# Performance work log

Measured on AMD Instinct MI355X. Metric: run time of the kernel, lower is better.

## Reference

```python
import jax, jax.numpy as jnp
import numpy as np

D_MODEL = 1024
N_HEADS = 16
HEAD_DIM = D_MODEL // N_HEADS
WINDOW = 256
NEG_INF = -1e30  # finite stand-in for -inf; identical softmax result, NaN-safe


def setup_inputs() -> dict:
    key = jax.random.key(0)
    ks = jax.random.split(key, 5)
    B, L = 1, 4096
    s = 1.0 / np.sqrt(D_MODEL)
    return {
        "x": jax.random.normal(ks[0], (B, L, D_MODEL), dtype=jnp.float32),
        "Wq": jax.random.normal(ks[1], (D_MODEL, D_MODEL), dtype=jnp.float32) * s,
        "Wk": jax.random.normal(ks[2], (D_MODEL, D_MODEL), dtype=jnp.float32) * s,
        "Wv": jax.random.normal(ks[3], (D_MODEL, D_MODEL), dtype=jnp.float32) * s,
        "Wo": jax.random.normal(ks[4], (D_MODEL, D_MODEL), dtype=jnp.float32) * s,
    }


def reference(x, Wq, Wk, Wv, Wo):
    B, L, _ = x.shape
    # projections (nn.Linear applies x @ W.T; weights here are stored as [out,in])
    q = (x @ Wq.T).reshape(B, L, N_HEADS, HEAD_DIM).transpose(0, 2, 1, 3)  # [B,H,L,Dh]
    k = (x @ Wk.T).reshape(B, L, N_HEADS, HEAD_DIM).transpose(0, 2, 1, 3)
    v = (x @ Wv.T).reshape(B, L, N_HEADS, HEAD_DIM).transpose(0, 2, 1, 3)

    # sliding-window causal mask: position i attends to j in [i-WINDOW+1, i]
    i = jnp.arange(L)[:, None]
    j = jnp.arange(L)[None, :]
    allowed = (j <= i) & (j >= i - WINDOW + 1)  # [L,L] bool

    scale = 1.0 / jnp.sqrt(jnp.asarray(HEAD_DIM, dtype=q.dtype))
    scores = jnp.einsum("bhqd,bhkd->bhqk", q, k) * scale  # [B,H,L,L]
    scores = jnp.where(allowed, scores, NEG_INF)
    attn = jax.nn.softmax(scores, axis=-1)
    out = jnp.einsum("bhqk,bhkd->bhqd", attn, v)  # [B,H,L,Dh]
    out = out.transpose(0, 2, 1, 3).reshape(B, L, D_MODEL)
    return out @ Wo.T
```

## Files before the change

kernel.cpp:

```cpp
#include <hip/hip_runtime.h>

using bf16x8 = __attribute__((ext_vector_type(8))) short;
using u16x8  = __attribute__((ext_vector_type(8))) unsigned short;
using f32x4  = __attribute__((ext_vector_type(4))) float;

#define LSEQ   4096
#define NH     16
#define DH     64
#define WIN    256
#define DM     1024

__device__ __forceinline__ void gl2lds16(const void* g, void* l) {
  __builtin_amdgcn_global_load_lds(
      (const __attribute__((address_space(1))) unsigned int*)g,
      (__attribute__((address_space(3))) unsigned int*)l,
      16, 0, 0);
}

__device__ __forceinline__ unsigned short f2bf(float f) {
  unsigned int u = __float_as_uint(f);
  u += 0x7fffu + ((u >> 16) & 1u);
  return (unsigned short)(u >> 16);
}

__global__ __launch_bounds__(256) void cvt_all(
    const float* __restrict__ x,  const float* __restrict__ wq,
    const float* __restrict__ wk, const float* __restrict__ wv,
    const float* __restrict__ wo, unsigned short* __restrict__ dst)
{
  const size_t i = ((size_t)blockIdx.x * 256 + threadIdx.x) * 8;
  const size_t XN = (size_t)LSEQ * DM;
  const float* src;
  size_t off;
  if (i < XN) { src = x; off = i; }
  else {
    const size_t j = i - XN;
    const int s = (int)(j >> 20);
    off = j & ((1u << 20) - 1);
    src = (s == 0) ? wq : (s == 1) ? wk : (s == 2) ? wv : wo;
  }
  const f32x4 f0 = *(const f32x4*)(src + off);
  const f32x4 f1 = *(const f32x4*)(src + off + 4);
  u16x8 o;
  o[0] = f2bf(f0[0]); o[1] = f2bf(f0[1]); o[2] = f2bf(f0[2]); o[3] = f2bf(f0[3]);
  o[4] = f2bf(f1[0]); o[5] = f2bf(f1[1]); o[6] = f2bf(f1[2]); o[7] = f2bf(f1[3]);
  *(u16x8*)(dst + i) = o;
}

__device__ __forceinline__ void gemm_tile(
    const unsigned short* __restrict__ X,
    const unsigned short* __restrict__ W,
    int m0, int n0,
    unsigned short* As, unsigned short* Bs,
    f32x4 (&acc)[4][4])
{
  const int tid  = threadIdx.x;
  const int lane = tid & 63;
  const int wave = tid >> 6;
  const int wm = wave >> 1, wn = wave & 1;
  const int fr = lane & 15, quad = lane >> 4;

  const f32x4 zero = {0.f, 0.f, 0.f, 0.f};
  #pragma unroll
  for (int i = 0; i < 4; ++i)
    #pragma unroll
    for (int j = 0; j < 4; ++j)
      acc[i][j] = zero;

  const unsigned short* ga[4];
  const unsigned short* gb[4];
  char* la[4];
  char* lb[4];
  #pragma unroll
  for (int cc = 0; cc < 4; ++cc) {
    const int c = tid + cc * 256;
    const int row = c >> 3;
    const int gp  = (c & 7) ^ (row & 7);
    ga[cc] = X + (size_t)(m0 + row) * DM + gp * 8;
    gb[cc] = W + (size_t)(n0 + row) * DM + gp * 8;
    la[cc] = (char*)As + c * 16;
    lb[cc] = (char*)Bs + c * 16;
  }

  const int sw = fr & 7;
  for (int kt = 0; kt < DM; kt += 64) {
    #pragma unroll
    for (int cc = 0; cc < 4; ++cc) {
      gl2lds16(ga[cc] + kt, la[cc]);
      gl2lds16(gb[cc] + kt, lb[cc]);
    }
    __syncthreads();

    #pragma unroll
    for (int s = 0; s < 2; ++s) {
      bf16x8 a[4], b[4];
      #pragma unroll
      for (int t = 0; t < 4; ++t)
        a[t] = *(const bf16x8*)(As + (wm * 64 + t * 16 + fr) * 64
                                   + (((s * 4 + quad) ^ sw) * 8));
      #pragma unroll
      for (int t = 0; t < 4; ++t)
        b[t] = *(const bf16x8*)(Bs + (wn * 64 + t * 16 + fr) * 64
                                   + (((s * 4 + quad) ^ sw) * 8));
      #pragma unroll
      for (int i = 0; i < 4; ++i)
        #pragma unroll
        for (int j = 0; j < 4; ++j)
          acc[i][j] = __builtin_amdgcn_mfma_f32_16x16x32_bf16(a[i], b[j], acc[i][j], 0, 0, 0);
    }
    __syncthreads();
  }
}

__global__ __launch_bounds__(256) void proj_gemm(
    const unsigned short* __restrict__ X,
    const unsigned short* __restrict__ Wq,
    const unsigned short* __restrict__ Wk,
    const unsigned short* __restrict__ Wv,
    unsigned short* __restrict__ Qo,
    unsigned short* __restrict__ Ko,
    unsigned short* __restrict__ Vt)
{
  __shared__ unsigned short As[128 * 64];
  __shared__ unsigned short Bs[128 * 64];
  const int id = blockIdx.x;
  const int lane = threadIdx.x & 63;
  const int wave = threadIdx.x >> 6;
  const int wm = wave >> 1, wn = wave & 1;
  const int cn = lane & 15, quad = lane >> 4;
  f32x4 acc[4][4];

  if (id < 512) {
    const int m0   = (id & 31) * 128;
    const int by   = id >> 5;
    const int wsel = by >> 3;
    const int n0   = (by & 7) * 128;
    gemm_tile(X, wsel ? Wk : Wq, m0, n0, As, Bs, acc);

    const float qscl = wsel ? 1.0f : 0.180336881f;
    unsigned short* O = wsel ? Ko : Qo;
    #pragma unroll
    for (int i = 0; i < 4; ++i)
      #pragma unroll
      for (int j = 0; j < 4; ++j)
        #pragma unroll
        for (int r = 0; r < 4; ++r) {
          const int row = m0 + wm * 64 + i * 16 + quad * 4 + r;
          const int col = n0 + wn * 64 + j * 16 + cn;
          const int h = col >> 6, d = col & 63;
          O[(size_t)(h * LSEQ + row) * DH + d] = f2bf(acc[i][j][r] * qscl);
        }
  } else {
    const int vid = id - 512;
    const int m0 = (vid & 7) * 128;
    const int n0 = (vid >> 3) * 128;
    gemm_tile(Wv, X, m0, n0, As, Bs, acc);

    #pragma unroll
    for (int i = 0; i < 4; ++i)
      #pragma unroll
      for (int j = 0; j < 4; ++j)
        #pragma unroll
        for (int r = 0; r < 4; ++r) {
          const int row = m0 + wm * 64 + i * 16 + quad * 4 + r;
          const int col = n0 + wn * 64 + j * 16 + cn;
          Vt[(size_t)row * LSEQ + col] = f2bf(acc[i][j][r]);
        }
  }
}

__global__ __launch_bounds__(256) void out_gemm(
    const unsigned short* __restrict__ X,
    const unsigned short* __restrict__ W,
    float* __restrict__ O)
{
  __shared__ unsigned short As2[64 * 64];
  __shared__ unsigned short Bs[128 * 64];
  const int m0 = blockIdx.x * 64;
  const int n0 = blockIdx.y * 128;
  const int tid  = threadIdx.x;
  const int lane = tid & 63;
  const int wave = tid >> 6;
  const int wm = wave >> 1, wn = wave & 1;
  const int fr = lane & 15, quad = lane >> 4;

  const f32x4 zero = {0.f, 0.f, 0.f, 0.f};
  f32x4 acc[2][4];
  #pragma unroll
  for (int i = 0; i < 2; ++i)
    #pragma unroll
    for (int j = 0; j < 4; ++j)
      acc[i][j] = zero;

  const unsigned short* ga[2];
  char* la[2];
  #pragma unroll
  for (int cc = 0; cc < 2; ++cc) {
    const int c = tid + cc * 256;
    const int row = c >> 3;
    const int gp  = (c & 7) ^ (row & 7);
    ga[cc] = X + (size_t)(m0 + row) * DM + gp * 8;
    la[cc] = (char*)As2 + c * 16;
  }
  const unsigned short* gb[4];
  char* lb[4];
  #pragma unroll
  for (int cc = 0; cc < 4; ++cc) {
    const int c = tid + cc * 256;
    const int row = c >> 3;
    const int gp  = (c & 7) ^ (row & 7);
    gb[cc] = W + (size_t)(n0 + row) * DM + gp * 8;
    lb[cc] = (char*)Bs + c * 16;
  }

  const int sw = fr & 7;
  for (int kt = 0; kt < DM; kt += 64) {
    #pragma unroll
    for (int cc = 0; cc < 2; ++cc)
      gl2lds16(ga[cc] + kt, la[cc]);
    #pragma unroll
    for (int cc = 0; cc < 4; ++cc)
      gl2lds16(gb[cc] + kt, lb[cc]);
    __syncthreads();

    #pragma unroll
    for (int s = 0; s < 2; ++s) {
      bf16x8 a[2], b[4];
      #pragma unroll
      for (int t = 0; t < 2; ++t)
        a[t] = *(const bf16x8*)(As2 + (wm * 32 + t * 16 + fr) * 64
                                    + (((s * 4 + quad) ^ sw) * 8));
      #pragma unroll
      for (int t = 0; t < 4; ++t)
        b[t] = *(const bf16x8*)(Bs + (wn * 64 + t * 16 + fr) * 64
                                   + (((s * 4 + quad) ^ sw) * 8));
      #pragma unroll
      for (int i = 0; i < 2; ++i)
        #pragma unroll
        for (int j = 0; j < 4; ++j)
          acc[i][j] = __builtin_amdgcn_mfma_f32_16x16x32_bf16(a[i], b[j], acc[i][j], 0, 0, 0);
    }
    __syncthreads();
  }

  const int cn = lane & 15;
  #pragma unroll
  for (int i = 0; i < 2; ++i)
    #pragma unroll
    for (int j = 0; j < 4; ++j)
      #pragma unroll
      for (int r = 0; r < 4; ++r) {
        const int row = m0 + wm * 32 + i * 16 + quad * 4 + r;
        const int col = n0 + wn * 64 + j * 16 + cn;
        O[(size_t)row * DM + col] = acc[i][j][r];
      }
}

#define PSTR 72
__global__ __launch_bounds__(512) void attn_fwd(
    const unsigned short* __restrict__ Q,
    const unsigned short* __restrict__ K,
    const unsigned short* __restrict__ Vt,
    unsigned short* __restrict__ Oa)
{
  __shared__ unsigned short Ks[2][64 * PSTR];
  __shared__ unsigned short Vs[2][64 * PSTR];
  __shared__ unsigned short Pl[8][16 * PSTR];
  const int id   = blockIdx.x;
  const int h    = (id & 7) | ((id >> 8) << 3);
  const int bq0  = ((id >> 3) & 31) * 128;
  const int tid  = threadIdx.x;
  const int wave = tid >> 6;
  const int lane = tid & 63;
  const int n = lane & 15, quad = lane >> 4;
  const int q0 = bq0 + wave * 16;
  unsigned short* pl = Pl[wave];

  const size_t qbase = ((size_t)(h * LSEQ + q0 + n)) * DH + quad * 8;
  const bf16x8 aq0 = *(const bf16x8*)(Q + qbase);
  const bf16x8 aq1 = *(const bf16x8*)(Q + qbase + 32);

  const int lo = (bq0 >= WIN) ? (bq0 - WIN) : 0;
  const int hi = bq0 + 128;

  const int krow = tid >> 3, part = tid & 7;
  const size_t kg = ((size_t)(h * LSEQ + krow)) * DH + part * 8;
  const size_t vg = ((size_t)(h * DH + krow)) * LSEQ + part * 8;
  const int ld = krow * PSTR + part * 8;

  {
    *(bf16x8*)(Ks[0] + ld) = *(const bf16x8*)(K  + kg + (size_t)lo * DH);
    *(bf16x8*)(Vs[0] + ld) = *(const bf16x8*)(Vt + vg + lo);
  }
  __syncthreads();

  const f32x4 zero = {0.f, 0.f, 0.f, 0.f};
  f32x4 acc[4] = {zero, zero, zero, zero};
  float li[4] = {0.f, 0.f, 0.f, 0.f};

  int t = 0;
  for (int jb = lo; jb < hi; jb += 64, ++t) {
    const int buf = t & 1;
    const bool more = (jb + 64 < hi);
    bf16x8 nk, nv;
    if (more) {
      nk = *(const bf16x8*)(K  + kg + (size_t)(jb + 64) * DH);
      nv = *(const bf16x8*)(Vt + vg + (jb + 64));
    }
    const bool active = (jb <= q0 + 15) && (jb + 63 >= q0 - (WIN - 1));
    if (active) {
      const unsigned short* ks = Ks[buf];
      const unsigned short* vs = Vs[buf];
      f32x4 s[4];
      __builtin_amdgcn_s_setprio(1);
      #pragma unroll
      for (int u = 0; u < 4; ++u) {
        const bf16x8 kb0 = *(const bf16x8*)(ks + (u * 16 + n) * PSTR + quad * 8);
        const bf16x8 kb1 = *(const bf16x8*)(ks + (u * 16 + n) * PSTR + 32 + quad * 8);
        f32x4 c = zero;
        c = __builtin_amdgcn_mfma_f32_16x16x32_bf16(aq0, kb0, c, 0, 0, 0);
        c = __builtin_amdgcn_mfma_f32_16x16x32_bf16(aq1, kb1, c, 0, 0, 0);
        s[u] = c;
      }
      __builtin_amdgcn_s_setprio(0);
      const bool nomask = (jb + 63 <= q0) && (jb >= q0 + 15 - (WIN - 1));
      if (nomask) {
        #pragma unroll
        for (int u = 0; u < 4; ++u)
          #pragma unroll
          for (int r = 0; r < 4; ++r) {
            const float e = __builtin_exp2f(s[u][r] - 32.0f);
            s[u][r] = e;
            li[r] += e;
          }
      } else {
        #pragma unroll
        for (int u = 0; u < 4; ++u)
          #pragma unroll
          for (int r = 0; r < 4; ++r) {
            const int qi = q0 + quad * 4 + r;
            const int kj = jb + u * 16 + n;
            const bool ok = (kj <= qi) && (kj + WIN > qi);
            const float e = __builtin_exp2f(ok ? s[u][r] - 32.0f : -1e30f);
            s[u][r] = e;
            li[r] += e;
          }
      }
      #pragma unroll
      for (int u = 0; u < 4; ++u)
        #pragma unroll
        for (int r = 0; r < 4; ++r)
          pl[(quad * 4 + r) * PSTR + u * 16 + n] = f2bf(s[u][r]);
      asm volatile("s_waitcnt lgkmcnt(0)" ::: "memory");
      const bf16x8 pa0 = *(const bf16x8*)(pl + n * PSTR + quad * 8);
      const bf16x8 pa1 = *(const bf16x8*)(pl + n * PSTR + 32 + quad * 8);
      __builtin_amdgcn_s_setprio(1);
      #pragma unroll
      for (int ct = 0; ct < 4; ++ct) {
        const bf16x8 vb0 = *(const bf16x8*)(vs + (ct * 16 + n) * PSTR + quad * 8);
        const bf16x8 vb1 = *(const bf16x8*)(vs + (ct * 16 + n) * PSTR + 32 + quad * 8);
        acc[ct] = __builtin_amdgcn_mfma_f32_16x16x32_bf16(pa0, vb0, acc[ct], 0, 0, 0);
        acc[ct] = __builtin_amdgcn_mfma_f32_16x16x32_bf16(pa1, vb1, acc[ct], 0, 0, 0);
      }
      __builtin_amdgcn_s_setprio(0);
    }
    if (more) {
      *(bf16x8*)(Ks[buf ^ 1] + ld) = nk;
      *(bf16x8*)(Vs[buf ^ 1] + ld) = nv;
    }
    __syncthreads();
  }

  float rd[4];
  #pragma unroll
  for (int r = 0; r < 4; ++r) {
    float v = li[r];
    v += __shfl_xor(v, 1);
    v += __shfl_xor(v, 2);
    v += __shfl_xor(v, 4);
    v += __shfl_xor(v, 8);
    rd[r] = 1.0f / v;
  }
  #pragma unroll
  for (int ct = 0; ct < 4; ++ct)
    #pragma unroll
    for (int r = 0; r < 4; ++r) {
      const int row = q0 + quad * 4 + r;
      const int col = h * DH + ct * 16 + n;
      Oa[(size_t)row * DM + col] = f2bf(acc[ct][r] * rd[r]);
    }
}

extern "C" void kernel_launch(void* const* d_in, const int* in_sizes, int n_in,
                              void* d_out, int out_size, void* d_ws, size_t ws_size,
                              hipStream_t stream) {
  const float* x  = (const float*)d_in[0];
  const float* Wq = (const float*)d_in[1];
  const float* Wk = (const float*)d_in[2];
  const float* Wv = (const float*)d_in[3];
  const float* Wo = (const float*)d_in[4];
  float* out = (float*)d_out;

  unsigned short* xb  = (unsigned short*)d_ws;
  unsigned short* Wqb = xb  + (size_t)LSEQ * DM;
  unsigned short* Wkb = Wqb + (size_t)DM * DM;
  unsigned short* Wvb = Wkb + (size_t)DM * DM;
  unsigned short* Wob = Wvb + (size_t)DM * DM;
  unsigned short* Q    = Wob + (size_t)DM * DM;
  unsigned short* K    = Q   + (size_t)LSEQ * DM;
  unsigned short* Vt   = K   + (size_t)LSEQ * DM;
  unsigned short* Attn = Vt  + (size_t)LSEQ * DM;

  cvt_all<<<dim3(4096), 256, 0, stream>>>(x, Wq, Wk, Wv, Wo, xb);
  proj_gemm<<<dim3(768), 256, 0, stream>>>(xb, Wqb, Wkb, Wvb, Q, K, Vt);
  attn_fwd<<<dim3(512), 512, 0, stream>>>(Q, K, Vt, Attn);
  out_gemm<<<dim3(64, 8), 256, 0, stream>>>(Attn, Wob, out);
}
```

Baseline: 154.4 us.

## Rewrite projection GEMM as 8-wave 256x256 tiles with double-buffered LDS pipeline

After: 155.3 us. About the same (+0.5%).

```diff
diff --git a/kernel.cpp b/kernel.cpp
--- a/kernel.cpp
+++ b/kernel.cpp
@@ -47,124 +47,189 @@
   *(u16x8*)(dst + i) = o;
 }
 
-__device__ __forceinline__ void gemm_tile(
+#define TS 16384
+
+#define RD_A(f, s, P) (*(const bf16x8*)(Ab + (P) + (wm*128 + (f)*16 + fr)*64 + ((((s)*4+quad) ^ swz)*8)))
+#define RD_B(g, s, P) (*(const bf16x8*)(Bb + (P) + (wn*64  + (g)*16 + fr)*64 + ((((s)*4+quad) ^ swz)*8)))
+
+#define QUAD16(fs, gs)                                                         \
+  do {                                                                         \
+    __builtin_amdgcn_s_setprio(1);                                             \
+    _Pragma("unroll")                                                          \
+    for (int f_ = 0; f_ < 4; ++f_)                                             \
+      _Pragma("unroll")                                                        \
+      for (int g_ = 0; g_ < 2; ++g_)                                           \
+        _Pragma("unroll")                                                      \
+        for (int s_ = 0; s_ < 2; ++s_)                                         \
+          acc[(fs)+f_][(gs)+g_] = __builtin_amdgcn_mfma_f32_16x16x32_bf16(     \
+              a[(fs)+f_][s_], b[(gs)+g_][s_], acc[(fs)+f_][(gs)+g_], 0, 0, 0); \
+    __builtin_amdgcn_s_setprio(0);                                             \
+  } while (0)
+
+__global__ __launch_bounds__(512, 2) void proj8(
     const unsigned short* __restrict__ X,
-    const unsigned short* __restrict__ W,
-    int m0, int n0,
-    unsigned short* As, unsigned short* Bs,
-    f32x4 (&acc)[4][4])
-{
-  const int tid  = threadIdx.x;
-  const int lane = tid & 63;
-  const int wave = tid >> 6;
-  const int wm = wave >> 1, wn = wave & 1;
-  const int fr = lane & 15, quad = lane >> 4;
-
-  const f32x4 zero = {0.f, 0.f, 0.f, 0.f};
-  #pragma unroll
-  for (int i = 0; i < 4; ++i)
-    #pragma unroll
-    for (int j = 0; j < 4; ++j)
-      acc[i][j] = zero;
-
-  const unsigned short* ga[4];
-  const unsigned short* gb[4];
-  char* la[4];
-  char* lb[4];
-  #pragma unroll
-  for (int cc = 0; cc < 4; ++cc) {
-    const int c = tid + cc * 256;
-    const int row = c >> 3;
-    const int gp  = (c & 7) ^ (row & 7);
-    ga[cc] = X + (size_t)(m0 + row) * DM + gp * 8;
-    gb[cc] = W + (size_t)(n0 + row) * DM + gp * 8;
-    la[cc] = (char*)As + c * 16;
-    lb[cc] = (char*)Bs + c * 16;
-  }
-
-  const int sw = fr & 7;
-  for (int kt = 0; kt < DM; kt += 64) {
-    #pragma unroll
-    for (int cc = 0; cc < 4; ++cc) {
-      gl2lds16(ga[cc] + kt, la[cc]);
-      gl2lds16(gb[cc] + kt, lb[cc]);
-    }
-    __syncthreads();
-
-    #pragma unroll
-    for (int s = 0; s < 2; ++s) {
-      bf16x8 a[4], b[4];
-      #pragma unroll
-      for (int t = 0; t < 4; ++t)
-        a[t] = *(const bf16x8*)(As + (wm * 64 + t * 16 + fr) * 64
-                                   + (((s * 4 + quad) ^ sw) * 8));
-      #pragma unroll
-      for (int t = 0; t < 4; ++t)
-        b[t] = *(const bf16x8*)(Bs + (wn * 64 + t * 16 + fr) * 64
-                                   + (((s * 4 + quad) ^ sw) * 8));
-      #pragma unroll
-      for (int i = 0; i < 4; ++i)
-        #pragma unroll
-        for (int j = 0; j < 4; ++j)
-          acc[i][j] = __builtin_amdgcn_mfma_f32_16x16x32_bf16(a[i], b[j], acc[i][j], 0, 0, 0);
-    }
-    __syncthreads();
-  }
-}
-
-__global__ __launch_bounds__(256) void proj_gemm(
-    const unsigned short* __restrict__ X,
-    const unsigned short* __restrict__ Wq,
-    const unsigned short* __restrict__ Wk,
+    const unsigned short* __restrict__ Wqk,
     const unsigned short* __restrict__ Wv,
     unsigned short* __restrict__ Qo,
     unsigned short* __restrict__ Ko,
     unsigned short* __restrict__ Vt)
 {
-  __shared__ unsigned short As[128 * 64];
-  __shared__ unsigned short Bs[128 * 64];
-  const int id = blockIdx.x;
-  const int lane = threadIdx.x & 63;
-  const int wave = threadIdx.x >> 6;
-  const int wm = wave >> 1, wn = wave & 1;
-  const int cn = lane & 15, quad = lane >> 4;
-  f32x4 acc[4][4];
-
-  if (id < 512) {
-    const int m0   = (id & 31) * 128;
-    const int by   = id >> 5;
-    const int wsel = by >> 3;
-    const int n0   = (by & 7) * 128;
-    gemm_tile(X, wsel ? Wk : Wq, m0, n0, As, Bs, acc);
-
-    const float qscl = wsel ? 1.0f : 0.180336881f;
-    unsigned short* O = wsel ? Ko : Qo;
-    #pragma unroll
-    for (int i = 0; i < 4; ++i)
-      #pragma unroll
-      for (int j = 0; j < 4; ++j)
+  __shared__ __align__(16) unsigned short Ab[2 * TS];
+  __shared__ __align__(16) unsigned short Bb[2 * TS];
+
+  const int id   = blockIdx.x;
+  const bool qk  = (id < 128);
+  const int tid  = threadIdx.x;
+  const int lane = tid & 63;
+  const int wave = tid >> 6;
+  const int wm   = wave >> 2;
+  const int wn   = wave & 3;
+  const int fr   = lane & 15, quad = lane >> 4;
+  const int swz  = fr & 7;
+
+  int m0, n0;
+  const unsigned short *Ag, *Bg;
+  if (qk) {
+    m0 = (id & 15) * 256;
+    n0 = (id >> 4) * 256;
+    Ag = X; Bg = Wqk;
+  } else {
+    const int v = id - 128;
+    m0 = (v & 3) * 256;
+    n0 = (v >> 2) * 256;
+    Ag = Wv; Bg = X;
+  }
+
+  const int crow = tid >> 3;
+  const int gp   = (tid & 7) ^ (crow & 7);
+  const unsigned short* gA0 = Ag + (size_t)(m0 + crow) * DM + gp * 8;
+  const unsigned short* gB0 = Bg + (size_t)(n0 + crow) * DM + gp * 8;
+  const int lc0 = tid * 8;
+
+  #define ST_A(t, g)                                                          \
+    do { if ((t) < 16) {                                                      \
+      const int p_ = ((t) & 1) * TS;                                          \
+      gl2lds16(gA0 + (2*(g))  * (64*DM) + (t)*64, (char*)(Ab + p_ + lc0 + (2*(g))  * 4096)); \
+      gl2lds16(gA0 + (2*(g)+1)* (64*DM) + (t)*64, (char*)(Ab + p_ + lc0 + (2*(g)+1)* 4096)); \
+    } } while (0)
+  #define ST_B(t, g)                                                          \
+    do { if ((t) < 16) {                                                      \
+      const int p_ = ((t) & 1) * TS;                                          \
+      gl2lds16(gB0 + (2*(g))  * (64*DM) + (t)*64, (char*)(Bb + p_ + lc0 + (2*(g))  * 4096)); \
+      gl2lds16(gB0 + (2*(g)+1)* (64*DM) + (t)*64, (char*)(Bb + p_ + lc0 + (2*(g)+1)* 4096)); \
+    } } while (0)
+
+  const f32x4 zero = {0.f, 0.f, 0.f, 0.f};
+  f32x4 acc[8][4];
+  #pragma unroll
+  for (int f = 0; f < 8; ++f)
+    #pragma unroll
+    for (int g = 0; g < 4; ++g)
+      acc[f][g] = zero;
+
+  bf16x8 a[8][2], b[4][2];
+
+  ST_A(0, 0); ST_A(0, 1); ST_B(0, 0); ST_B(0, 1);
+  ST_A(1, 0); ST_A(1, 1);
+  asm volatile("s_waitcnt vmcnt(4)" ::: "memory");
+  __builtin_amdgcn_s_barrier();
+
+  for (int i = 0; i < 8; ++i) {
+    const int T1 = 2*i + 1, T2 = 2*i + 2, T3 = 2*i + 3;
+
+    #pragma unroll
+    for (int f = 0; f < 4; ++f) { a[f][0] = RD_A(f, 0, 0); a[f][1] = RD_A(f, 1, 0); }
+    #pragma unroll
+    for (int g = 0; g < 2; ++g) { b[g][0] = RD_B(g, 0, 0); b[g][1] = RD_B(g, 1, 0); }
+    ST_B(T1, 0);
+    __builtin_amdgcn_s_barrier();
+    asm volatile("s_waitcnt lgkmcnt(0)" ::: "memory");
+    QUAD16(0, 0);
+    __builtin_amdgcn_s_barrier();
+
+    #pragma unroll
+    for (int f = 4; f < 8; ++f) { a[f][0] = RD_A(f, 0, 0); a[f][1] = RD_A(f, 1, 0); }
+    #pragma unroll
+    for (int g = 2; g < 4; ++g) { b[g][0] = RD_B(g, 0, 0); b[g][1] = RD_B(g, 1, 0); }
+    ST_B(T1, 1);
+    __builtin_amdgcn_s_barrier();
+    asm volatile("s_waitcnt lgkmcnt(0)" ::: "memory");
+    QUAD16(4, 0);
+    __builtin_amdgcn_sched_barrier(0);
+    __builtin_amdgcn_s_barrier();
+
+    ST_A(T2, 0);
+    __builtin_amdgcn_s_barrier();
+    QUAD16(0, 2);
+    __builtin_amdgcn_s_barrier();
+
+    ST_A(T2, 1);
+    __builtin_amdgcn_s_barrier();
+    QUAD16(4, 2);
+    if (i == 7) asm volatile("s_waitcnt vmcnt(0)" ::: "memory");
+    else        asm volatile("s_waitcnt vmcnt(4)" ::: "memory");
+    __builtin_amdgcn_s_barrier();
+
+    #pragma unroll
+    for (int f = 0; f < 4; ++f) { a[f][0] = RD_A(f, 0, TS); a[f][1] = RD_A(f, 1, TS); }
+    #pragma unroll
+    for (int g = 0; g < 2; ++g) { b[g][0] = RD_B(g, 0, TS); b[g][1] = RD_B(g, 1, TS); }
+    ST_B(T2, 0);
+    __builtin_amdgcn_s_barrier();
+    asm volatile("s_waitcnt lgkmcnt(0)" ::: "memory");
+    QUAD16(0, 0);
+    __builtin_amdgcn_s_barrier();
+
+    #pragma unroll
+    for (int f = 4; f < 8; ++f) { a[f][0] = RD_A(f, 0, TS); a[f][1] = RD_A(f, 1, TS); }
+    #pragma unroll
+    for (int g = 2; g < 4; ++g) { b[g][0] = RD_B(g, 0, TS); b[g][1] = RD_B(g, 1, TS); }
+    ST_B(T2, 1);
+    __builtin_amdgcn_s_barrier();
+    asm volatile("s_waitcnt lgkmcnt(0)" ::: "memory");
+    QUAD16(4, 0);
+    __builtin_amdgcn_sched_barrier(0);
+    __builtin_amdgcn_s_barrier();
+
+    ST_A(T3, 0);
+    __builtin_amdgcn_s_barrier();
+    QUAD16(0, 2);
+    __builtin_amdgcn_s_barrier();
+
+    ST_A(T3, 1);
+    __builtin_amdgcn_s_barrier();
+    QUAD16(4, 2);
+    if (i < 7) asm volatile("s_waitcnt vmcnt(4)" ::: "memory");
+    __builtin_amdgcn_s_barrier();
+  }
+
+  const int cn = fr;
+  if (qk) {
+    const bool isK = (n0 >= 1024);
+    const float qscl = isK ? 1.0f : 0.180336881f;
+    unsigned short* O = isK ? Ko : Qo;
+    const int nb = isK ? (n0 - 1024) : n0;
+    #pragma unroll
+    for (int f = 0; f < 8; ++f)
+      #pragma unroll
+      for (int g = 0; g < 4; ++g)
         #pragma unroll
         for (int r = 0; r < 4; ++r) {
-          const int row = m0 + wm * 64 + i * 16 + quad * 4 + r;
-          const int col = n0 + wn * 64 + j * 16 + cn;
+          const int row = m0 + wm * 128 + f * 16 + quad * 4 + r;
+          const int col = nb + wn * 64 + g * 16 + cn;
           const int h = col >> 6, d = col & 63;
-          O[(size_t)(h * LSEQ + row) * DH + d] = f2bf(acc[i][j][r] * qscl);
+          O[(size_t)(h * LSEQ + row) * DH + d] = f2bf(acc[f][g][r] * qscl);
         }
   } else {
-    const int vid = id - 512;
-    const int m0 = (vid & 7) * 128;
-    const int n0 = (vid >> 3) * 128;
-    gemm_tile(Wv, X, m0, n0, As, Bs, acc);
-
-    #pragma unroll
-    for (int i = 0; i < 4; ++i)
-      #pragma unroll
-      for (int j = 0; j < 4; ++j)
+    #pragma unroll
+    for (int f = 0; f < 8; ++f)
+      #pragma unroll
+      for (int g = 0; g < 4; ++g)
         #pragma unroll
         for (int r = 0; r < 4; ++r) {
-          const int row = m0 + wm * 64 + i * 16 + quad * 4 + r;
-          const int col = n0 + wn * 64 + j * 16 + cn;
-          Vt[(size_t)row * LSEQ + col] = f2bf(acc[i][j][r]);
+          const int row = m0 + wm * 128 + f * 16 + quad * 4 + r;
+          const int col = n0 + wn * 64 + g * 16 + cn;
+          Vt[(size_t)row * LSEQ + col] = f2bf(acc[f][g][r]);
         }
   }
 }
@@ -198,8 +263,8 @@
   for (int cc = 0; cc < 2; ++cc) {
     const int c = tid + cc * 256;
     const int row = c >> 3;
-    const int gp  = (c & 7) ^ (row & 7);
-    ga[cc] = X + (size_t)(m0 + row) * DM + gp * 8;
+    const int gpp = (c & 7) ^ (row & 7);
+    ga[cc] = X + (size_t)(m0 + row) * DM + gpp * 8;
     la[cc] = (char*)As2 + c * 16;
   }
   const unsigned short* gb[4];
@@ -208,8 +273,8 @@
   for (int cc = 0; cc < 4; ++cc) {
     const int c = tid + cc * 256;
     const int row = c >> 3;
-    const int gp  = (c & 7) ^ (row & 7);
-    gb[cc] = W + (size_t)(n0 + row) * DM + gp * 8;
+    const int gpp = (c & 7) ^ (row & 7);
+    gb[cc] = W + (size_t)(n0 + row) * DM + gpp * 8;
     lb[cc] = (char*)Bs + c * 16;
   }
 
@@ -412,7 +477,7 @@
   unsigned short* Attn = Vt  + (size_t)LSEQ * DM;
 
   cvt_all<<<dim3(4096), 256, 0, stream>>>(x, Wq, Wk, Wv, Wo, xb);
-  proj_gemm<<<dim3(768), 256, 0, stream>>>(xb, Wqb, Wkb, Wvb, Q, K, Vt);
+  proj8<<<dim3(192), 512, 0, stream>>>(xb, Wqb, Wvb, Q, K, Vt);
   attn_fwd<<<dim3(512), 512, 0, stream>>>(Q, K, Vt, Attn);
   out_gemm<<<dim3(64, 8), 256, 0, stream>>>(Attn, Wob, out);
 }
```

## Enlarge projection GEMM tiles to 256x128 with 512-thread blocks and MFMA priority

Applied to the files above, without the earlier changes.

After: 166.5 us. 7.8% more time.

```diff
diff --git a/kernel.cpp b/kernel.cpp
--- a/kernel.cpp
+++ b/kernel.cpp
@@ -47,124 +47,127 @@
   *(u16x8*)(dst + i) = o;
 }
 
-__device__ __forceinline__ void gemm_tile(
+__global__ __launch_bounds__(512) void proj2(
     const unsigned short* __restrict__ X,
-    const unsigned short* __restrict__ W,
-    int m0, int n0,
-    unsigned short* As, unsigned short* Bs,
-    f32x4 (&acc)[4][4])
-{
-  const int tid  = threadIdx.x;
-  const int lane = tid & 63;
-  const int wave = tid >> 6;
-  const int wm = wave >> 1, wn = wave & 1;
-  const int fr = lane & 15, quad = lane >> 4;
-
-  const f32x4 zero = {0.f, 0.f, 0.f, 0.f};
-  #pragma unroll
-  for (int i = 0; i < 4; ++i)
-    #pragma unroll
-    for (int j = 0; j < 4; ++j)
-      acc[i][j] = zero;
-
-  const unsigned short* ga[4];
-  const unsigned short* gb[4];
-  char* la[4];
-  char* lb[4];
-  #pragma unroll
-  for (int cc = 0; cc < 4; ++cc) {
-    const int c = tid + cc * 256;
-    const int row = c >> 3;
-    const int gp  = (c & 7) ^ (row & 7);
-    ga[cc] = X + (size_t)(m0 + row) * DM + gp * 8;
-    gb[cc] = W + (size_t)(n0 + row) * DM + gp * 8;
-    la[cc] = (char*)As + c * 16;
-    lb[cc] = (char*)Bs + c * 16;
-  }
-
-  const int sw = fr & 7;
-  for (int kt = 0; kt < DM; kt += 64) {
-    #pragma unroll
-    for (int cc = 0; cc < 4; ++cc) {
-      gl2lds16(ga[cc] + kt, la[cc]);
-      gl2lds16(gb[cc] + kt, lb[cc]);
-    }
-    __syncthreads();
-
-    #pragma unroll
-    for (int s = 0; s < 2; ++s) {
-      bf16x8 a[4], b[4];
-      #pragma unroll
-      for (int t = 0; t < 4; ++t)
-        a[t] = *(const bf16x8*)(As + (wm * 64 + t * 16 + fr) * 64
-                                   + (((s * 4 + quad) ^ sw) * 8));
-      #pragma unroll
-      for (int t = 0; t < 4; ++t)
-        b[t] = *(const bf16x8*)(Bs + (wn * 64 + t * 16 + fr) * 64
-                                   + (((s * 4 + quad) ^ sw) * 8));
-      #pragma unroll
-      for (int i = 0; i < 4; ++i)
-        #pragma unroll
-        for (int j = 0; j < 4; ++j)
-          acc[i][j] = __builtin_amdgcn_mfma_f32_16x16x32_bf16(a[i], b[j], acc[i][j], 0, 0, 0);
-    }
-    __syncthreads();
-  }
-}
-
-__global__ __launch_bounds__(256) void proj_gemm(
-    const unsigned short* __restrict__ X,
-    const unsigned short* __restrict__ Wq,
-    const unsigned short* __restrict__ Wk,
+    const unsigned short* __restrict__ Wqk,
     const unsigned short* __restrict__ Wv,
     unsigned short* __restrict__ Qo,
     unsigned short* __restrict__ Ko,
     unsigned short* __restrict__ Vt)
 {
-  __shared__ unsigned short As[128 * 64];
-  __shared__ unsigned short Bs[128 * 64];
-  const int id = blockIdx.x;
-  const int lane = threadIdx.x & 63;
-  const int wave = threadIdx.x >> 6;
-  const int wm = wave >> 1, wn = wave & 1;
-  const int cn = lane & 15, quad = lane >> 4;
+  __shared__ __align__(16) unsigned short As[256 * 64];
+  __shared__ __align__(16) unsigned short Bs[128 * 64];
+
+  const int id   = blockIdx.x;
+  const bool qk  = (id < 256);
+  const int tid  = threadIdx.x;
+  const int lane = tid & 63;
+  const int wave = tid >> 6;
+  const int wm   = wave >> 1;
+  const int wn   = wave & 1;
+  const int fr   = lane & 15, quad = lane >> 4;
+  const int swz  = fr & 7;
+
+  int m0, n0;
+  const unsigned short *Ag, *Bg;
+  if (qk) {
+    m0 = (id & 15) * 256;
+    n0 = (id >> 4) * 128;
+    Ag = X; Bg = Wqk;
+  } else {
+    const int v = id - 256;
+    m0 = (v & 3) * 256;
+    n0 = (v >> 2) * 128;
+    Ag = Wv; Bg = X;
+  }
+
+  const f32x4 zero = {0.f, 0.f, 0.f, 0.f};
   f32x4 acc[4][4];
-
-  if (id < 512) {
-    const int m0   = (id & 31) * 128;
-    const int by   = id >> 5;
-    const int wsel = by >> 3;
-    const int n0   = (by & 7) * 128;
-    gemm_tile(X, wsel ? Wk : Wq, m0, n0, As, Bs, acc);
-
-    const float qscl = wsel ? 1.0f : 0.180336881f;
-    unsigned short* O = wsel ? Ko : Qo;
-    #pragma unroll
-    for (int i = 0; i < 4; ++i)
-      #pragma unroll
-      for (int j = 0; j < 4; ++j)
+  #pragma unroll
+  for (int f = 0; f < 4; ++f)
+    #pragma unroll
+    for (int g = 0; g < 4; ++g)
+      acc[f][g] = zero;
+
+  const unsigned short* ga[4];
+  char* la[4];
+  #pragma unroll
+  for (int cc = 0; cc < 4; ++cc) {
+    const int c = tid + cc * 512;
+    const int row = c >> 3;
+    const int gp  = (c & 7) ^ (row & 7);
+    ga[cc] = Ag + (size_t)(m0 + row) * DM + gp * 8;
+    la[cc] = (char*)As + c * 16;
+  }
+  const unsigned short* gb[2];
+  char* lb[2];
+  #pragma unroll
+  for (int cc = 0; cc < 2; ++cc) {
+    const int c = tid + cc * 512;
+    const int row = c >> 3;
+    const int gp  = (c & 7) ^ (row & 7);
+    gb[cc] = Bg + (size_t)(n0 + row) * DM + gp * 8;
+    lb[cc] = (char*)Bs + c * 16;
+  }
+
+  for (int kt = 0; kt < DM; kt += 64) {
+    #pragma unroll
+    for (int cc = 0; cc < 4; ++cc)
+      gl2lds16(ga[cc] + kt, la[cc]);
+    #pragma unroll
+    for (int cc = 0; cc < 2; ++cc)
+      gl2lds16(gb[cc] + kt, lb[cc]);
+    __syncthreads();
+
+    #pragma unroll
+    for (int s = 0; s < 2; ++s) {
+      bf16x8 a[4], b[4];
+      #pragma unroll
+      for (int t = 0; t < 4; ++t)
+        a[t] = *(const bf16x8*)(As + (wm * 64 + t * 16 + fr) * 64
+                                   + (((s * 4 + quad) ^ swz) * 8));
+      #pragma unroll
+      for (int t = 0; t < 4; ++t)
+        b[t] = *(const bf16x8*)(Bs + (wn * 64 + t * 16 + fr) * 64
+                                   + (((s * 4 + quad) ^ swz) * 8));
+      __builtin_amdgcn_s_setprio(1);
+      #pragma unroll
+      for (int i = 0; i < 4; ++i)
+        #pragma unroll
+        for (int j = 0; j < 4; ++j)
+          acc[i][j] = __builtin_amdgcn_mfma_f32_16x16x32_bf16(a[i], b[j], acc[i][j], 0, 0, 0);
+      __builtin_amdgcn_s_setprio(0);
+    }
+    __syncthreads();
+  }
+
+  const int cn = fr;
+  if (qk) {
+    const bool isK = (n0 >= 1024);
+    const float qscl = isK ? 1.0f : 0.180336881f;
+    unsigned short* O = isK ? Ko : Qo;
+    const int nb = isK ? (n0 - 1024) : n0;
+    #pragma unroll
+    for (int f = 0; f < 4; ++f)
+      #pragma unroll
+      for (int g = 0; g < 4; ++g)
         #pragma unroll
         for (int r = 0; r < 4; ++r) {
-          const int row = m0 + wm * 64 + i * 16 + quad * 4 + r;
-          const int col = n0 + wn * 64 + j * 16 + cn;
+          const int row = m0 + wm * 64 + f * 16 + quad * 4 + r;
+          const int col = nb + wn * 64 + g * 16 + cn;
           const int h = col >> 6, d = col & 63;
-          O[(size_t)(h * LSEQ + row) * DH + d] = f2bf(acc[i][j][r] * qscl);
+          O[(size_t)(h * LSEQ + row) * DH + d] = f2bf(acc[f][g][r] * qscl);
         }
   } else {
-    const int vid = id - 512;
-    const int m0 = (vid & 7) * 128;
-    const int n0 = (vid >> 3) * 128;
-    gemm_tile(Wv, X, m0, n0, As, Bs, acc);
-
-    #pragma unroll
-    for (int i = 0; i < 4; ++i)
-      #pragma unroll
-      for (int j = 0; j < 4; ++j)
+    #pragma unroll
+    for (int f = 0; f < 4; ++f)
+      #pragma unroll
+      for (int g = 0; g < 4; ++g)
         #pragma unroll
         for (int r = 0; r < 4; ++r) {
-          const int row = m0 + wm * 64 + i * 16 + quad * 4 + r;
-          const int col = n0 + wn * 64 + j * 16 + cn;
-          Vt[(size_t)row * LSEQ + col] = f2bf(acc[i][j][r]);
+          const int row = m0 + wm * 64 + f * 16 + quad * 4 + r;
+          const int col = n0 + wn * 64 + g * 16 + cn;
+          Vt[(size_t)row * LSEQ + col] = f2bf(acc[f][g][r]);
         }
   }
 }
@@ -198,8 +201,8 @@
   for (int cc = 0; cc < 2; ++cc) {
     const int c = tid + cc * 256;
     const int row = c >> 3;
-    const int gp  = (c & 7) ^ (row & 7);
-    ga[cc] = X + (size_t)(m0 + row) * DM + gp * 8;
+    const int gpp = (c & 7) ^ (row & 7);
+    ga[cc] = X + (size_t)(m0 + row) * DM + gpp * 8;
     la[cc] = (char*)As2 + c * 16;
   }
   const unsigned short* gb[4];
@@ -208,8 +211,8 @@
   for (int cc = 0; cc < 4; ++cc) {
     const int c = tid + cc * 256;
     const int row = c >> 3;
-    const int gp  = (c & 7) ^ (row & 7);
-    gb[cc] = W + (size_t)(n0 + row) * DM + gp * 8;
+    const int gpp = (c & 7) ^ (row & 7);
+    gb[cc] = W + (size_t)(n0 + row) * DM + gpp * 8;
     lb[cc] = (char*)Bs + c * 16;
   }
 
@@ -412,7 +415,7 @@
   unsigned short* Attn = Vt  + (size_t)LSEQ * DM;
 
   cvt_all<<<dim3(4096), 256, 0, stream>>>(x, Wq, Wk, Wv, Wo, xb);
-  proj_gemm<<<dim3(768), 256, 0, stream>>>(xb, Wqb, Wkb, Wvb, Q, K, Vt);
+  proj2<<<dim3(384), 512, 0, stream>>>(xb, Wqb, Wvb, Q, K, Vt);
   attn_fwd<<<dim3(512), 512, 0, stream>>>(Q, K, Vt, Attn);
   out_gemm<<<dim3(64, 8), 256, 0, stream>>>(Attn, Wob, out);
 }
```

## Double-buffer LDS tiles in projection GEMM to overlap loads with MFMA

Applied to the files above, without the earlier changes.

Measured after the change: 152.8 us. No clear change (-1.1%).

```diff
diff --git a/kernel.cpp b/kernel.cpp
--- a/kernel.cpp
+++ b/kernel.cpp
@@ -47,11 +47,11 @@
   *(u16x8*)(dst + i) = o;
 }
 
-__device__ __forceinline__ void gemm_tile(
+__device__ __forceinline__ void gemm_tile_db(
     const unsigned short* __restrict__ X,
     const unsigned short* __restrict__ W,
     int m0, int n0,
-    unsigned short* As, unsigned short* Bs,
+    unsigned short* As0, unsigned short* Bs0,
     f32x4 (&acc)[4][4])
 {
   const int tid  = threadIdx.x;
@@ -59,6 +59,7 @@
   const int wave = tid >> 6;
   const int wm = wave >> 1, wn = wave & 1;
   const int fr = lane & 15, quad = lane >> 4;
+  const int sw = fr & 7;
 
   const f32x4 zero = {0.f, 0.f, 0.f, 0.f};
   #pragma unroll
@@ -69,8 +70,7 @@
 
   const unsigned short* ga[4];
   const unsigned short* gb[4];
-  char* la[4];
-  char* lb[4];
+  int lc[4];
   #pragma unroll
   for (int cc = 0; cc < 4; ++cc) {
     const int c = tid + cc * 256;
@@ -78,38 +78,58 @@
     const int gp  = (c & 7) ^ (row & 7);
     ga[cc] = X + (size_t)(m0 + row) * DM + gp * 8;
     gb[cc] = W + (size_t)(n0 + row) * DM + gp * 8;
-    la[cc] = (char*)As + c * 16;
-    lb[cc] = (char*)Bs + c * 16;
-  }
-
-  const int sw = fr & 7;
-  for (int kt = 0; kt < DM; kt += 64) {
-    #pragma unroll
-    for (int cc = 0; cc < 4; ++cc) {
-      gl2lds16(ga[cc] + kt, la[cc]);
-      gl2lds16(gb[cc] + kt, lb[cc]);
-    }
-    __syncthreads();
-
-    #pragma unroll
-    for (int s = 0; s < 2; ++s) {
-      bf16x8 a[4], b[4];
-      #pragma unroll
-      for (int t = 0; t < 4; ++t)
-        a[t] = *(const bf16x8*)(As + (wm * 64 + t * 16 + fr) * 64
-                                   + (((s * 4 + quad) ^ sw) * 8));
-      #pragma unroll
-      for (int t = 0; t < 4; ++t)
-        b[t] = *(const bf16x8*)(Bs + (wn * 64 + t * 16 + fr) * 64
-                                   + (((s * 4 + quad) ^ sw) * 8));
-      #pragma unroll
-      for (int i = 0; i < 4; ++i)
-        #pragma unroll
-        for (int j = 0; j < 4; ++j)
-          acc[i][j] = __builtin_amdgcn_mfma_f32_16x16x32_bf16(a[i], b[j], acc[i][j], 0, 0, 0);
-    }
-    __syncthreads();
-  }
+    lc[cc] = c * 16;
+  }
+  char* laA = (char*)As0;
+  char* laB = (char*)Bs0;
+
+  #pragma unroll
+  for (int cc = 0; cc < 4; ++cc) {
+    gl2lds16(ga[cc], laA + lc[cc]);
+    gl2lds16(gb[cc], laB + lc[cc]);
+  }
+  __syncthreads();
+
+  #define PITER(KT, CUR, NXT)                                                 \
+    do {                                                                      \
+      if ((KT) + 64 < DM) {                                                   \
+        _Pragma("unroll")                                                     \
+        for (int cc = 0; cc < 4; ++cc) {                                      \
+          gl2lds16(ga[cc] + (KT) + 64, laA + (NXT) * 16384 + lc[cc]);         \
+          gl2lds16(gb[cc] + (KT) + 64, laB + (NXT) * 16384 + lc[cc]);         \
+        }                                                                     \
+      }                                                                       \
+      const unsigned short* As_ = As0 + (CUR) * 8192;                         \
+      const unsigned short* Bs_ = Bs0 + (CUR) * 8192;                         \
+      _Pragma("unroll")                                                       \
+      for (int s = 0; s < 2; ++s) {                                           \
+        bf16x8 a[4], b[4];                                                    \
+        _Pragma("unroll")                                                     \
+        for (int t = 0; t < 4; ++t)                                           \
+          a[t] = *(const bf16x8*)(As_ + (wm * 64 + t * 16 + fr) * 64          \
+                                      + (((s * 4 + quad) ^ sw) * 8));         \
+        _Pragma("unroll")                                                     \
+        for (int t = 0; t < 4; ++t)                                           \
+          b[t] = *(const bf16x8*)(Bs_ + (wn * 64 + t * 16 + fr) * 64          \
+                                      + (((s * 4 + quad) ^ sw) * 8));         \
+        __builtin_amdgcn_s_setprio(1);                                        \
+        _Pragma("unroll")                                                     \
+        for (int i = 0; i < 4; ++i)                                           \
+          _Pragma("unroll")                                                   \
+          for (int j = 0; j < 4; ++j)                                         \
+            acc[i][j] = __builtin_amdgcn_mfma_f32_16x16x32_bf16(              \
+                a[i], b[j], acc[i][j], 0, 0, 0);                              \
+        __builtin_amdgcn_s_setprio(0);                                        \
+      }                                                                       \
+      __syncthreads();                                                        \
+    } while (0)
+
+  #pragma unroll 1
+  for (int kt2 = 0; kt2 < DM; kt2 += 128) {
+    PITER(kt2,      0, 1);
+    PITER(kt2 + 64, 1, 0);
+  }
+  #undef PITER
 }
 
 __global__ __launch_bounds__(256) void proj_gemm(
@@ -121,8 +141,8 @@
     unsigned short* __restrict__ Ko,
     unsigned short* __restrict__ Vt)
 {
-  __shared__ unsigned short As[128 * 64];
-  __shared__ unsigned short Bs[128 * 64];
+  __shared__ __align__(16) unsigned short As[2 * 128 * 64];
+  __shared__ __align__(16) unsigned short Bs[2 * 128 * 64];
   const int id = blockIdx.x;
   const int lane = threadIdx.x & 63;
   const int wave = threadIdx.x >> 6;
@@ -135,7 +155,7 @@
     const int by   = id >> 5;
     const int wsel = by >> 3;
     const int n0   = (by & 7) * 128;
-    gemm_tile(X, wsel ? Wk : Wq, m0, n0, As, Bs, acc);
+    gemm_tile_db(X, wsel ? Wk : Wq, m0, n0, As, Bs, acc);
 
     const float qscl = wsel ? 1.0f : 0.180336881f;
     unsigned short* O = wsel ? Ko : Qo;
@@ -154,7 +174,7 @@
     const int vid = id - 512;
     const int m0 = (vid & 7) * 128;
     const int n0 = (vid >> 3) * 128;
-    gemm_tile(Wv, X, m0, n0, As, Bs, acc);
+    gemm_tile_db(Wv, X, m0, n0, As, Bs, acc);
 
     #pragma unroll
     for (int i = 0; i < 4; ++i)
@@ -198,8 +218,8 @@
   for (int cc = 0; cc < 2; ++cc) {
     const int c = tid + cc * 256;
     const int row = c >> 3;
-    const int gp  = (c & 7) ^ (row & 7);
-    ga[cc] = X + (size_t)(m0 + row) * DM + gp * 8;
+    const int gpp = (c & 7) ^ (row & 7);
+    ga[cc] = X + (size_t)(m0 + row) * DM + gpp * 8;
     la[cc] = (char*)As2 + c * 16;
   }
   const unsigned short* gb[4];
@@ -208,8 +228,8 @@
   for (int cc = 0; cc < 4; ++cc) {
     const int c = tid + cc * 256;
     const int row = c >> 3;
-    const int gp  = (c & 7) ^ (row & 7);
-    gb[cc] = W + (size_t)(n0 + row) * DM + gp * 8;
+    const int gpp = (c & 7) ^ (row & 7);
+    gb[cc] = W + (size_t)(n0 + row) * DM + gpp * 8;
     lb[cc] = (char*)Bs + c * 16;
   }
 
```
